# Optimization experiments

Hardware: AMD Instinct MI355X
Metric: run time of the kernel (lower is better)

The kernel has to match this reference:

```python
import jax, jax.numpy as jnp
import numpy as np

D_MODEL = 1024
NHEAD = 16
HEAD_DIM = D_MODEL // NHEAD
EPS = 1e-5


def _layer_norm(x, gamma, beta):
    mu = jnp.mean(x, axis=-1, keepdims=True)
    var = jnp.mean(jnp.square(x - mu), axis=-1, keepdims=True)
    return (x - mu) * jax.lax.rsqrt(var + EPS) * gamma + beta


def setup_inputs() -> dict:
    key = jax.random.key(0)
    ks = jax.random.split(key, 8)
    s = 1.0 / np.sqrt(D_MODEL)
    return {
        "x": jax.random.normal(ks[0], (4, 2048, D_MODEL), dtype=jnp.float32),
        "Wq": jax.random.uniform(ks[1], (D_MODEL, D_MODEL), jnp.float32, -s, s),
        "Wk": jax.random.uniform(ks[2], (D_MODEL, D_MODEL), jnp.float32, -s, s),
        "Wv": jax.random.uniform(ks[3], (D_MODEL, D_MODEL), jnp.float32, -s, s),
        "ln1_g": jnp.ones((D_MODEL,), jnp.float32),
        "ln1_b": jnp.zeros((D_MODEL,), jnp.float32),
        "ln2_g": jnp.ones((D_MODEL,), jnp.float32),
        "ln2_b": jnp.zeros((D_MODEL,), jnp.float32),
        "W1": jax.random.uniform(ks[4], (D_MODEL, D_MODEL), jnp.float32, -s, s),
        "b1": jax.random.uniform(ks[5], (D_MODEL,), jnp.float32, -s, s),
        "W2": jax.random.uniform(ks[6], (D_MODEL, D_MODEL), jnp.float32, -s, s),
        "b2": jax.random.uniform(ks[7], (D_MODEL,), jnp.float32, -s, s),
    }


def reference(x, Wq, Wk, Wv, ln1_g, ln1_b, ln2_g, ln2_b, W1, b1, W2, b2):
    B, S, D = x.shape
    temperature = jnp.sqrt(jnp.asarray(D_MODEL / NHEAD, x.dtype))
    xn = _layer_norm(x, ln1_g, ln1_b)
    # torch Linear: y = x @ W.T (weights are [out, in], no bias for q/k/v)
    q = (xn @ Wq.T).reshape(B, S, NHEAD, HEAD_DIM)
    k = (xn @ Wk.T).reshape(B, S, NHEAD, HEAD_DIM)
    v = (xn @ Wv.T).reshape(B, S, NHEAD, HEAD_DIM)
    scores = jnp.einsum("bqhd,bkhd->bhqk", q, k) / temperature  # [B,H,S,S]
    causal = jnp.tril(jnp.ones((S, S), dtype=bool))
    scores = jnp.where(causal, scores, jnp.asarray(-jnp.inf, scores.dtype))
    attn = jax.nn.softmax(scores, axis=-1)
    att_out = jnp.einsum("bhqk,bkhd->bqhd", attn, v).reshape(B, S, D)
    xt = x + att_out
    xt2 = _layer_norm(xt, ln2_g, ln2_b)
    ffn = jax.nn.relu(xt2 @ W1.T + b1) @ W2.T + b2  # dropout=0 -> identity
    return xt + ffn
```

## Files before the change

### kernel.cpp

```cpp
#include <hip/hip_runtime.h>
#include <hip/hip_bf16.h>

typedef unsigned short u16;
typedef unsigned int u32;
typedef __attribute__((ext_vector_type(8))) __bf16 bf16x8;
typedef __attribute__((ext_vector_type(4))) float f32x4;
typedef __attribute__((ext_vector_type(16))) float f32x16;
typedef __attribute__((ext_vector_type(8))) unsigned short ushort8v;
typedef __attribute__((ext_vector_type(4))) unsigned short u16x4;
typedef __attribute__((ext_vector_type(4))) unsigned int u32x4;

#define DEV __device__ __forceinline__
#define AS1 __attribute__((address_space(1)))
#define AS3 __attribute__((address_space(3)))

DEV u16 f2bf(float f) {
    union { float f; unsigned int i; } u; u.f = f;
    unsigned int x = u.i;
    unsigned int r = (x + 0x7fffu + ((x >> 16) & 1u)) >> 16;
    return (u16)r;
}
DEV float bf2f(u16 h) {
    union { unsigned int i; float f; } u; u.i = ((unsigned int)h) << 16;
    return u.f;
}
DEV u32 cvt_pk_bf16(float lo, float hi) {
    u32 r;
    asm("v_cvt_pk_bf16_f32 %0, %1, %2" : "=v"(r) : "v"(lo), "v"(hi));
    return r;
}
DEV void pl32swap(u32& a, u32& b) {
    asm volatile("v_permlane32_swap_b32 %0, %1" : "+v"(a), "+v"(b));
}

__global__ __launch_bounds__(256) void ln1_cvt(
    const float* __restrict__ xin,
    const float* __restrict__ g, const float* __restrict__ be,
    u16* __restrict__ y_bf,
    const float* __restrict__ wq, const float* __restrict__ wk,
    const float* __restrict__ wv, const float* __restrict__ w1,
    const float* __restrict__ w2, u16* __restrict__ wdst)
{
    const int tid = threadIdx.x;
    if (blockIdx.x >= 8192) {
        const int i = ((blockIdx.x - 8192) * 256 + tid) * 4;
        auto conv4 = [](float4 a, float s) {
            u16x4 r; r[0] = f2bf(a.x * s); r[1] = f2bf(a.y * s);
            r[2] = f2bf(a.z * s); r[3] = f2bf(a.w * s);
            return r;
        };
        const float qs = 0.125f * 1.44269504f;
        *(u16x4*)(wdst + i)               = conv4(*(const float4*)(wq + i), qs);
        *(u16x4*)(wdst + (1 << 20) + i)   = conv4(*(const float4*)(wk + i), 1.0f);
        *(u16x4*)(wdst + (2 << 20) + i)   = conv4(*(const float4*)(wv + i), 1.0f);
        *(u16x4*)(wdst + (3 << 20) + i)   = conv4(*(const float4*)(w1 + i), 1.0f);
        *(u16x4*)(wdst + (4 << 20) + i)   = conv4(*(const float4*)(w2 + i), 1.0f);
        return;
    }
    const int row = blockIdx.x;
    const size_t base = (size_t)row * 1024 + tid * 4;
    float4 xv = *(const float4*)(xin + base);
    float v[4] = {xv.x, xv.y, xv.z, xv.w};
    float s = 0.f, ss = 0.f;
    #pragma unroll
    for (int j = 0; j < 4; ++j) { s += v[j]; ss += v[j] * v[j]; }
    #pragma unroll
    for (int o = 32; o > 0; o >>= 1) { s += __shfl_xor(s, o); ss += __shfl_xor(ss, o); }
    __shared__ float red[8];
    const int w = tid >> 6;
    if ((tid & 63) == 0) { red[w * 2] = s; red[w * 2 + 1] = ss; }
    __syncthreads();
    s  = red[0] + red[2] + red[4] + red[6];
    ss = red[1] + red[3] + red[5] + red[7];
    const float mu = s * (1.0f / 1024.0f);
    const float var = ss * (1.0f / 1024.0f) - mu * mu;
    const float rstd = rsqrtf(var + 1e-5f);
    const int col = tid * 4;
    float4 gv = *(const float4*)(g + col);
    float4 bv = *(const float4*)(be + col);
    u16x4 o4;
    o4[0] = f2bf((v[0] - mu) * rstd * gv.x + bv.x);
    o4[1] = f2bf((v[1] - mu) * rstd * gv.y + bv.y);
    o4[2] = f2bf((v[2] - mu) * rstd * gv.z + bv.z);
    o4[3] = f2bf((v[3] - mu) * rstd * gv.w + bv.w);
    *(u16x4*)(y_bf + base) = o4;
}

__global__ __launch_bounds__(256) void ln2_kernel(
    const float* __restrict__ xin, const u16* __restrict__ addbf,
    const float* __restrict__ g, const float* __restrict__ be,
    u16* __restrict__ xt_out, u16* __restrict__ y_bf)
{
    const int row = blockIdx.x;
    const int tid = threadIdx.x;
    const size_t base = (size_t)row * 1024 + tid * 4;

    float4 xv = *(const float4*)(xin + base);
    float v[4] = {xv.x, xv.y, xv.z, xv.w};
    u16x4 a = *(const u16x4*)(addbf + base);
    v[0] += bf2f(a[0]); v[1] += bf2f(a[1]); v[2] += bf2f(a[2]); v[3] += bf2f(a[3]);
    u16x4 o;
    o[0] = f2bf(v[0]); o[1] = f2bf(v[1]); o[2] = f2bf(v[2]); o[3] = f2bf(v[3]);
    *(u16x4*)(xt_out + base) = o;

    float s = 0.f, ss = 0.f;
    #pragma unroll
    for (int j = 0; j < 4; ++j) { s += v[j]; ss += v[j] * v[j]; }
    #pragma unroll
    for (int o2 = 32; o2 > 0; o2 >>= 1) { s += __shfl_xor(s, o2); ss += __shfl_xor(ss, o2); }
    __shared__ float red[8];
    const int w = tid >> 6;
    if ((tid & 63) == 0) { red[w * 2] = s; red[w * 2 + 1] = ss; }
    __syncthreads();
    s  = red[0] + red[2] + red[4] + red[6];
    ss = red[1] + red[3] + red[5] + red[7];
    const float mu = s * (1.0f / 1024.0f);
    const float var = ss * (1.0f / 1024.0f) - mu * mu;
    const float rstd = rsqrtf(var + 1e-5f);

    const int col = tid * 4;
    float4 gv = *(const float4*)(g + col);
    float4 bv = *(const float4*)(be + col);
    u16x4 o4;
    o4[0] = f2bf((v[0] - mu) * rstd * gv.x + bv.x);
    o4[1] = f2bf((v[1] - mu) * rstd * gv.y + bv.y);
    o4[2] = f2bf((v[2] - mu) * rstd * gv.z + bv.z);
    o4[3] = f2bf((v[3] - mu) * rstd * gv.w + bv.w);
    *(u16x4*)(y_bf + base) = o4;
}

template<int EPI>
__global__ __launch_bounds__(256, 4) void gemm_bt(
    const u16* __restrict__ A, const u16* __restrict__ Bt,
    void* __restrict__ Cout, const float* __restrict__ bias,
    const u16* __restrict__ resid, int M, int N, int K)
{
    __shared__ u16 As[2 * 128 * 32];
    __shared__ u16 Bs[2 * 128 * 32];
    const int tid = threadIdx.x;
    const int l = tid & 63;
    const int w = tid >> 6;
    const int wm = w >> 1, wn = w & 1;
    const int fr = l & 15, fc = l >> 4;
    const size_t rowA0 = (size_t)blockIdx.x * 128;
    const size_t rowB0 = (size_t)blockIdx.y * 128;

    f32x4 acc[4][4] = {};
    const int ldoff = fr * 32 + fc * 8;

    const int nkt = K >> 6;
    for (int kt = 0; kt < nkt; ++kt) {
        __syncthreads();
        const int k0 = kt << 6;
        #pragma unroll
        for (int q = 0; q < 4; ++q) {
            const int row = (q & 1) * 64 + w * 16 + (l >> 2);
            const int kk  = (q >> 1) * 32 + (l & 3) * 8;
            const u16* ga = A  + (rowA0 + row) * K + k0 + kk;
            const u16* gb = Bt + (rowB0 + row) * K + k0 + kk;
            u16* da = As + q * 2048 + w * 512;
            u16* db = Bs + q * 2048 + w * 512;
            __builtin_amdgcn_global_load_lds((const AS1 void*)ga, (AS3 void*)da, 16, 0, 0);
            __builtin_amdgcn_global_load_lds((const AS1 void*)gb, (AS3 void*)db, 16, 0, 0);
        }
        __syncthreads();
        #pragma unroll
        for (int ks = 0; ks < 2; ++ks) {
            const u16* as_p = As + ks * 4096;
            const u16* bs_p = Bs + ks * 4096;
            bf16x8 af[4], bfv[4];
            #pragma unroll
            for (int m = 0; m < 4; ++m)
                af[m] = *(const bf16x8*)(as_p + (wm * 64 + m * 16) * 32 + ldoff);
            #pragma unroll
            for (int n = 0; n < 4; ++n)
                bfv[n] = *(const bf16x8*)(bs_p + (wn * 64 + n * 16) * 32 + ldoff);
            #pragma unroll
            for (int m = 0; m < 4; ++m)
                #pragma unroll
                for (int n = 0; n < 4; ++n)
                    acc[m][n] = __builtin_amdgcn_mfma_f32_16x16x32_bf16(
                        af[m], bfv[n], acc[m][n], 0, 0, 0);
        }
    }

    const int r0 = (int)rowA0 + wm * 64;
    const int c0 = (int)rowB0 + wn * 64;
    #pragma unroll
    for (int m = 0; m < 4; ++m) {
        #pragma unroll
        for (int n = 0; n < 4; ++n) {
            const int rowbase = r0 + m * 16 + fc * 4;
            const int col = c0 + n * 16 + fr;
            if constexpr (EPI == 0) {
                const int which = col >> 10;
                const int hh = (col >> 6) & 15;
                const int dd = col & 63;
                const size_t hb2 = (size_t)(rowbase >> 11) * 16 + hh;
                const int s0 = rowbase & 2047;
                if (which == 2) {
                    u16x4 pk;
                    #pragma unroll
                    for (int j = 0; j < 4; ++j) pk[j] = f2bf(acc[m][n][j]);
                    *(u16x4*)((u16*)Cout + (size_t)2 * 8388608 +
                              (hb2 * 64 + dd) * 2048 + s0) = pk;
                } else {
                    #pragma unroll
                    for (int j = 0; j < 4; ++j)
                        ((u16*)Cout)[(size_t)which * 8388608 +
                                     (hb2 * 2048 + s0 + j) * 64 + dd] =
                            f2bf(acc[m][n][j]);
                }
            } else {
                #pragma unroll
                for (int j = 0; j < 4; ++j) {
                    float v = acc[m][n][j];
                    const size_t idx = (size_t)(rowbase + j) * N + col;
                    if constexpr (EPI == 1) {
                        v += bias[col];
                        v = fmaxf(v, 0.0f);
                        ((u16*)Cout)[idx] = f2bf(v);
                    } else {
                        v += bias[col] + bf2f(resid[idx]);
                        ((float*)Cout)[idx] = v;
                    }
                }
            }
        }
    }
}

__global__ __launch_bounds__(256, 4) void attn_fwd(
    const u16* __restrict__ Qh, const u16* __restrict__ Kh,
    const u16* __restrict__ Vh, u16* __restrict__ attout)
{
    __shared__ u16 Ks[2][64 * 64];
    __shared__ u16 Vt[2][64 * 64];

    const int bid = blockIdx.x;
    const int pair = (bid >> 3) & 15;
    const int g = (bid & 7) + 8 * (bid >> 7);
    const int h = g & 15, b = g >> 4;

    const int tid = threadIdx.x, l = tid & 63, w = tid >> 6;
    const int lq = l & 31, hi = l >> 5, hi8 = hi * 8;
    const int qhalf = w & 1, kvblk = w >> 1;
    const int kvb32 = kvblk * 32;
    const int hb = b * 16 + h;
    const size_t head = (size_t)hb << 17;
    const u16* kb_g = Kh + head;
    const u16* vb_g = Vh + head;

    const int swr = (lq & 7) << 3;

    const int grow0 = w * 16 + (l >> 3);
    const int gsw   = ((l & 7) * 8) ^ ((l >> 3) << 3);

    #pragma unroll 1
    for (int half = 0; half < 2; ++half) {
        const int qt = half ? 31 - pair : pair;
        const int qbw = qt * 64 + qhalf * 32;
        const int qg = qbw + lq;

        bf16x8 qf[4];
        {
            const u16* qp = Qh + head + (size_t)(qbw + lq) * 64 + hi8;
            #pragma unroll
            for (int ds = 0; ds < 4; ++ds)
                qf[ds] = *(const bf16x8*)(qp + ds * 16);
        }

        f32x16 acc[2] = {};
        float l_part = 0.0f;

        const int nkt = qt + 1;
        int cur = 0;

        #pragma unroll
        for (int i = 0; i < 2; ++i) {
            const int row = grow0 + i * 8;
            __builtin_amdgcn_global_load_lds(
                (const AS1 void*)(kb_g + (size_t)row * 64 + gsw),
                (AS3 void*)(&Ks[0][0] + (w * 16 + i * 8) * 64), 16, 0, 0);
            __builtin_amdgcn_global_load_lds(
                (const AS1 void*)(vb_g + (size_t)row * 2048 + gsw),
                (AS3 void*)(&Vt[0][0] + (w * 16 + i * 8) * 64), 16, 0, 0);
        }
        __builtin_amdgcn_sched_barrier(0);
        asm volatile("s_waitcnt vmcnt(0)" ::: "memory");
        __builtin_amdgcn_s_barrier();

        #pragma unroll 1
        for (int kt = 0; kt < nkt; ++kt) {
            const int kv0 = kt * 64;
            const bool diag = (kt == qt);
            const u16* ksc = &Ks[cur][0];
            const u16* vtc = &Vt[cur][0];

            if (kt + 1 < nkt) {
                u16* ksn = &Ks[cur ^ 1][0];
                u16* vtn = &Vt[cur ^ 1][0];
                #pragma unroll
                for (int i = 0; i < 2; ++i) {
                    const int row = grow0 + i * 8;
                    __builtin_amdgcn_global_load_lds(
                        (const AS1 void*)(kb_g + (size_t)(kv0 + 64 + row) * 64 + gsw),
                        (AS3 void*)(ksn + (w * 16 + i * 8) * 64), 16, 0, 0);
                    __builtin_amdgcn_global_load_lds(
                        (const AS1 void*)(vb_g + (size_t)row * 2048 + kv0 + 64 + gsw),
                        (AS3 void*)(vtn + (w * 16 + i * 8) * 64), 16, 0, 0);
                }
            }
            __builtin_amdgcn_sched_barrier(0);

            if (!(diag && qhalf == 0 && kvblk == 1)) {
                f32x16 sa = {};
                const u16* kbase = ksc + (kvb32 + lq) * 64;
                __builtin_amdgcn_s_setprio(1);
                #pragma unroll
                for (int ds = 0; ds < 4; ++ds) {
                    const bf16x8 kf = *(const bf16x8*)(kbase + ((ds * 16 + hi8) ^ swr));
                    sa = __builtin_amdgcn_mfma_f32_32x32x16_bf16(kf, qf[ds], sa, 0, 0, 0);
                }
                __builtin_amdgcn_s_setprio(0);

                if (diag && kvblk == qhalf) {
                    const int kvbase = kv0 + kvb32 + 4 * hi;
                    #pragma unroll
                    for (int r = 0; r < 16; ++r) {
                        const int kg = kvbase + (r & 3) + 8 * (r >> 2);
                        if (kg > qg) sa[r] = -3.0e38f;
                    }
                }

                float ls = 0.0f;
                #pragma unroll
                for (int r = 0; r < 16; ++r) { sa[r] = exp2f(sa[r]); ls += sa[r]; }
                l_part += ls;

                u32 P0 = cvt_pk_bf16(sa[0],  sa[1]);
                u32 P1 = cvt_pk_bf16(sa[2],  sa[3]);
                u32 P2 = cvt_pk_bf16(sa[4],  sa[5]);
                u32 P3 = cvt_pk_bf16(sa[6],  sa[7]);
                u32 P4 = cvt_pk_bf16(sa[8],  sa[9]);
                u32 P5 = cvt_pk_bf16(sa[10], sa[11]);
                u32 P6 = cvt_pk_bf16(sa[12], sa[13]);
                u32 P7 = cvt_pk_bf16(sa[14], sa[15]);
                pl32swap(P0, P2); pl32swap(P1, P3);
                pl32swap(P4, P6); pl32swap(P5, P7);
                u32x4 w0v = {P0, P1, P2, P3};
                u32x4 w1v = {P4, P5, P6, P7};
                const bf16x8 pf0 = __builtin_bit_cast(bf16x8, w0v);
                const bf16x8 pf1 = __builtin_bit_cast(bf16x8, w1v);

                __builtin_amdgcn_s_setprio(1);
                #pragma unroll
                for (int dblk = 0; dblk < 2; ++dblk) {
                    const u16* vbase = vtc + (lq + dblk * 32) * 64;
                    const bf16x8 vf0 = *(const bf16x8*)(vbase + ((kvb32 + hi8) ^ swr));
                    acc[dblk] = __builtin_amdgcn_mfma_f32_32x32x16_bf16(
                        vf0, pf0, acc[dblk], 0, 0, 0);
                    const bf16x8 vf1 = *(const bf16x8*)(vbase + ((kvb32 + 16 + hi8) ^ swr));
                    acc[dblk] = __builtin_amdgcn_mfma_f32_32x32x16_bf16(
                        vf1, pf1, acc[dblk], 0, 0, 0);
                }
                __builtin_amdgcn_s_setprio(0);
            }

            __builtin_amdgcn_sched_barrier(0);
            asm volatile("s_waitcnt vmcnt(0)" ::: "memory");
            asm volatile("s_waitcnt lgkmcnt(0)" ::: "memory");
            __builtin_amdgcn_s_barrier();
            cur ^= 1;
        }

        float* accs = (float*)&Ks[0][0];
        float* lsh  = (float*)&Vt[0][0];
        if (kvblk == 1) {
            float* rgn = accs + qhalf * 2048;
            #pragma unroll
            for (int e = 0; e < 16; ++e) {
                rgn[e * 64 + l]        = acc[0][e];
                rgn[(16 + e) * 64 + l] = acc[1][e];
            }
            lsh[qhalf * 64 + l] = l_part;
        }
        __syncthreads();
        if (kvblk == 0) {
            const float* rgn = accs + qhalf * 2048;
            #pragma unroll
            for (int e = 0; e < 16; ++e) {
                acc[0][e] += rgn[e * 64 + l];
                acc[1][e] += rgn[(16 + e) * 64 + l];
            }
            l_part += lsh[qhalf * 64 + l];
            const float l_tot = l_part + __shfl_xor(l_part, 32);
            const float inv = 1.0f / l_tot;
            const size_t obase = ((size_t)b * 2048 + qbw + lq) * 1024 + h * 64;
            #pragma unroll
            for (int dblk = 0; dblk < 2; ++dblk) {
                #pragma unroll
                for (int gq = 0; gq < 4; ++gq) {
                    u16x4 o;
                    #pragma unroll
                    for (int j = 0; j < 4; ++j)
                        o[j] = f2bf(acc[dblk][4 * gq + j] * inv);
                    *(u16x4*)(attout + obase + dblk * 32 + gq * 8 + 4 * hi) = o;
                }
            }
        }
        __syncthreads();
    }
}

extern "C" void kernel_launch(void* const* d_in, const int* in_sizes, int n_in,
                              void* d_out, int out_size, void* d_ws, size_t ws_size,
                              hipStream_t stream)
{
    const float* x    = (const float*)d_in[0];
    const float* Wq   = (const float*)d_in[1];
    const float* Wk   = (const float*)d_in[2];
    const float* Wv   = (const float*)d_in[3];
    const float* ln1g = (const float*)d_in[4];
    const float* ln1b = (const float*)d_in[5];
    const float* ln2g = (const float*)d_in[6];
    const float* ln2b = (const float*)d_in[7];
    const float* W1   = (const float*)d_in[8];
    const float* b1   = (const float*)d_in[9];
    const float* W2   = (const float*)d_in[10];
    const float* b2   = (const float*)d_in[11];

    char* ws = (char*)d_ws;
    u16*   wbf  = (u16*)(ws);
    u16*   xn   = (u16*)(ws + 10485760);
    u16*   qkvb = (u16*)(ws + 27262976);
    u16*   attb = (u16*)(ws + 77594624);
    u16*   xt   = (u16*)(ws + 94371840);

    ln1_cvt<<<9216, 256, 0, stream>>>(x, ln1g, ln1b, xn, Wq, Wk, Wv, W1, W2, wbf);
    gemm_bt<0><<<dim3(64, 24), 256, 0, stream>>>(xn, wbf, qkvb, nullptr, nullptr,
                                                 8192, 3072, 1024);
    attn_fwd<<<1024, 256, 0, stream>>>(qkvb, qkvb + 8388608, qkvb + 16777216, attb);
    ln2_kernel<<<8192, 256, 0, stream>>>(x, attb, ln2g, ln2b, xt, xn);
    gemm_bt<1><<<dim3(64, 8), 256, 0, stream>>>(xn, wbf + (3 << 20), qkvb, b1, nullptr,
                                                8192, 1024, 1024);
    gemm_bt<2><<<dim3(64, 8), 256, 0, stream>>>(qkvb, wbf + (4 << 20), d_out, b2, xt,
                                                8192, 1024, 1024);
}
```

Before: 208.0 us.

## Use 64-row tiles for FFN GEMMs and compute softmax row sums via MFMA

Makes the GEMM kernel's M tile size a template parameter and launches the two FFN GEMMs with 64-row tiles, doubling their block count from 512 to 1024 so more blocks fill the GPU. Separately, the attention kernel no longer accumulates softmax denominators with scalar adds and a cross-lane shuffle. It now multiplies the probability fragments by a ones vector with two extra MFMAs per tile. The smaller tiles reduce data reuse per block, and the ones-MFMA adds matrix work and an extra 16-float accumulator, raising register pressure.

```diff
diff --git a/kernel.cpp b/kernel.cpp
--- a/kernel.cpp
+++ b/kernel.cpp
@@ -129,54 +129,72 @@
     *(u16x4*)(y_bf + base) = o4;
 }
 
-template<int EPI>
+template<int EPI, int BM>
 __global__ __launch_bounds__(256, 4) void gemm_bt(
     const u16* __restrict__ A, const u16* __restrict__ Bt,
     void* __restrict__ Cout, const float* __restrict__ bias,
     const u16* __restrict__ resid, int M, int N, int K)
 {
-    __shared__ u16 As[2 * 128 * 32];
+    constexpr int WM = BM / 2;
+    constexpr int MR = WM / 16;
+    __shared__ u16 As[2 * BM * 32];
     __shared__ u16 Bs[2 * 128 * 32];
     const int tid = threadIdx.x;
     const int l = tid & 63;
     const int w = tid >> 6;
     const int wm = w >> 1, wn = w & 1;
     const int fr = l & 15, fc = l >> 4;
-    const size_t rowA0 = (size_t)blockIdx.x * 128;
+    const size_t rowA0 = (size_t)blockIdx.x * BM;
     const size_t rowB0 = (size_t)blockIdx.y * 128;
 
-    f32x4 acc[4][4] = {};
+    f32x4 acc[MR][4] = {};
     const int ldoff = fr * 32 + fc * 8;
 
     const int nkt = K >> 6;
     for (int kt = 0; kt < nkt; ++kt) {
         __syncthreads();
         const int k0 = kt << 6;
+        if constexpr (BM == 128) {
+            #pragma unroll
+            for (int q = 0; q < 4; ++q) {
+                const int row = (q & 1) * 64 + w * 16 + (l >> 2);
+                const int kk  = (q >> 1) * 32 + (l & 3) * 8;
+                __builtin_amdgcn_global_load_lds(
+                    (const AS1 void*)(A + (rowA0 + row) * K + k0 + kk),
+                    (AS3 void*)(As + q * 2048 + w * 512), 16, 0, 0);
+            }
+        } else {
+            #pragma unroll
+            for (int q = 0; q < 2; ++q) {
+                const int row = w * 16 + (l >> 2);
+                const int kk  = q * 32 + (l & 3) * 8;
+                __builtin_amdgcn_global_load_lds(
+                    (const AS1 void*)(A + (rowA0 + row) * K + k0 + kk),
+                    (AS3 void*)(As + q * 2048 + w * 512), 16, 0, 0);
+            }
+        }
         #pragma unroll
         for (int q = 0; q < 4; ++q) {
             const int row = (q & 1) * 64 + w * 16 + (l >> 2);
             const int kk  = (q >> 1) * 32 + (l & 3) * 8;
-            const u16* ga = A  + (rowA0 + row) * K + k0 + kk;
-            const u16* gb = Bt + (rowB0 + row) * K + k0 + kk;
-            u16* da = As + q * 2048 + w * 512;
-            u16* db = Bs + q * 2048 + w * 512;
-            __builtin_amdgcn_global_load_lds((const AS1 void*)ga, (AS3 void*)da, 16, 0, 0);
-            __builtin_amdgcn_global_load_lds((const AS1 void*)gb, (AS3 void*)db, 16, 0, 0);
+            __builtin_amdgcn_global_load_lds(
+                (const AS1 void*)(Bt + (rowB0 + row) * K + k0 + kk),
+                (AS3 void*)(Bs + q * 2048 + w * 512), 16, 0, 0);
         }
         __syncthreads();
         #pragma unroll
         for (int ks = 0; ks < 2; ++ks) {
-            const u16* as_p = As + ks * 4096;
+            const u16* as_p = As + ks * (BM * 32);
             const u16* bs_p = Bs + ks * 4096;
-            bf16x8 af[4], bfv[4];
-            #pragma unroll
-            for (int m = 0; m < 4; ++m)
-                af[m] = *(const bf16x8*)(as_p + (wm * 64 + m * 16) * 32 + ldoff);
+            bf16x8 af[MR], bfv[4];
+            #pragma unroll
+            for (int m = 0; m < MR; ++m)
+                af[m] = *(const bf16x8*)(as_p + (wm * WM + m * 16) * 32 + ldoff);
             #pragma unroll
             for (int n = 0; n < 4; ++n)
                 bfv[n] = *(const bf16x8*)(bs_p + (wn * 64 + n * 16) * 32 + ldoff);
             #pragma unroll
-            for (int m = 0; m < 4; ++m)
+            for (int m = 0; m < MR; ++m)
                 #pragma unroll
                 for (int n = 0; n < 4; ++n)
                     acc[m][n] = __builtin_amdgcn_mfma_f32_16x16x32_bf16(
@@ -184,10 +202,10 @@
         }
     }
 
-    const int r0 = (int)rowA0 + wm * 64;
+    const int r0 = (int)rowA0 + wm * WM;
     const int c0 = (int)rowB0 + wn * 64;
     #pragma unroll
-    for (int m = 0; m < 4; ++m) {
+    for (int m = 0; m < MR; ++m) {
         #pragma unroll
         for (int n = 0; n < 4; ++n) {
             const int rowbase = r0 + m * 16 + fc * 4;
@@ -256,6 +274,10 @@
     const int grow0 = w * 16 + (l >> 3);
     const int gsw   = ((l & 7) * 8) ^ ((l >> 3) << 3);
 
+    bf16x8 onesv;
+    #pragma unroll
+    for (int j = 0; j < 8; ++j) onesv[j] = (__bf16)1.0f;
+
     #pragma unroll 1
     for (int half = 0; half < 2; ++half) {
         const int qt = half ? 31 - pair : pair;
@@ -271,7 +293,7 @@
         }
 
         f32x16 acc[2] = {};
-        float l_part = 0.0f;
+        f32x16 acc_l = {};
 
         const int nkt = qt + 1;
         int cur = 0;
@@ -333,10 +355,8 @@
                     }
                 }
 
-                float ls = 0.0f;
-                #pragma unroll
-                for (int r = 0; r < 16; ++r) { sa[r] = exp2f(sa[r]); ls += sa[r]; }
-                l_part += ls;
+                #pragma unroll
+                for (int r = 0; r < 16; ++r) sa[r] = exp2f(sa[r]);
 
                 u32 P0 = cvt_pk_bf16(sa[0],  sa[1]);
                 u32 P1 = cvt_pk_bf16(sa[2],  sa[3]);
@@ -364,6 +384,8 @@
                     acc[dblk] = __builtin_amdgcn_mfma_f32_32x32x16_bf16(
                         vf1, pf1, acc[dblk], 0, 0, 0);
                 }
+                acc_l = __builtin_amdgcn_mfma_f32_32x32x16_bf16(onesv, pf0, acc_l, 0, 0, 0);
+                acc_l = __builtin_amdgcn_mfma_f32_32x32x16_bf16(onesv, pf1, acc_l, 0, 0, 0);
                 __builtin_amdgcn_s_setprio(0);
             }
 
@@ -374,6 +396,8 @@
             cur ^= 1;
         }
 
+        float l_part = acc_l[0];
+
         float* accs = (float*)&Ks[0][0];
         float* lsh  = (float*)&Vt[0][0];
         if (kvblk == 1) {
@@ -394,7 +418,7 @@
                 acc[1][e] += rgn[(16 + e) * 64 + l];
             }
             l_part += lsh[qhalf * 64 + l];
-            const float l_tot = l_part + __shfl_xor(l_part, 32);
+            const float l_tot = l_part;
             const float inv = 1.0f / l_tot;
             const size_t obase = ((size_t)b * 2048 + qbw + lq) * 1024 + h * 64;
             #pragma unroll
@@ -438,12 +462,12 @@
     u16*   xt   = (u16*)(ws + 94371840);
 
     ln1_cvt<<<9216, 256, 0, stream>>>(x, ln1g, ln1b, xn, Wq, Wk, Wv, W1, W2, wbf);
-    gemm_bt<0><<<dim3(64, 24), 256, 0, stream>>>(xn, wbf, qkvb, nullptr, nullptr,
-                                                 8192, 3072, 1024);
+    gemm_bt<0, 128><<<dim3(64, 24), 256, 0, stream>>>(xn, wbf, qkvb, nullptr, nullptr,
+                                                      8192, 3072, 1024);
     attn_fwd<<<1024, 256, 0, stream>>>(qkvb, qkvb + 8388608, qkvb + 16777216, attb);
     ln2_kernel<<<8192, 256, 0, stream>>>(x, attb, ln2g, ln2b, xt, xn);
-    gemm_bt<1><<<dim3(64, 8), 256, 0, stream>>>(xn, wbf + (3 << 20), qkvb, b1, nullptr,
-                                                8192, 1024, 1024);
-    gemm_bt<2><<<dim3(64, 8), 256, 0, stream>>>(qkvb, wbf + (4 << 20), d_out, b2, xt,
-                                                8192, 1024, 1024);
-}
+    gemm_bt<1, 64><<<dim3(128, 8), 256, 0, stream>>>(xn, wbf + (3 << 20), qkvb, b1,
+                                                     nullptr, 8192, 1024, 1024);
+    gemm_bt<2, 64><<<dim3(128, 8), 256, 0, stream>>>(qkvb, wbf + (4 << 20), d_out, b2,
+                                                     xt, 8192, 1024, 1024);
+}
```

New measurement: 217.6 us. 4.6% more time.
